# Optimization experiments

Hardware: AMD Instinct MI355X
Metric: run time of the kernel (lower is better)

Reference implementation:

```python
import jax, jax.numpy as jnp
import numpy as np

N = 8192
D = 1024
TIME_DECAY = 86400.0
EPS = 1e-10


def setup_inputs() -> dict:
    key = jax.random.key(0)
    ks = jax.random.split(key, 8)
    x = jax.random.normal(ks[0], (N, D), dtype=jnp.float32)
    # timestamps spanning ~10 days so decay bias is non-trivial
    timestamps = jax.random.uniform(ks[1], (N,), dtype=jnp.float32) * (10.0 * TIME_DECAY)
    s = 1.0 / np.sqrt(D)
    Wq = jax.random.normal(ks[2], (D, D), dtype=jnp.float32) * s
    bq = jnp.zeros((D,), dtype=jnp.float32)
    Wk = jax.random.normal(ks[3], (D, D), dtype=jnp.float32) * s
    bk = jnp.zeros((D,), dtype=jnp.float32)
    Wv = jax.random.normal(ks[4], (D, D), dtype=jnp.float32) * s
    bv = jnp.zeros((D,), dtype=jnp.float32)
    return {"x": x, "timestamps": timestamps, "Wq": Wq, "bq": bq,
            "Wk": Wk, "bk": bk, "Wv": Wv, "bv": bv}


def reference(x, timestamps, Wq, bq, Wk, bk, Wv, bv):
    scale = jnp.asarray(D ** 0.5, x.dtype)
    # torch nn.Linear: y = x @ W.T + b
    Q = x @ Wq.T + bq          # [N, D]
    K = x @ Wk.T + bk          # [N, D]
    V = x @ Wv.T + bv          # [N, D]
    time_diff = timestamps[:, None] - timestamps[None, :]   # [N, N]
    time_decay = jnp.exp(-jnp.abs(time_diff) / TIME_DECAY)  # [N, N]
    scores = (Q @ K.T) / scale + jnp.log(time_decay + EPS)  # [N, N]
    attn = jax.nn.softmax(scores, axis=-1)
    return attn @ V
```

## Files before the change

### kernel.cpp

```cpp
#include <hip/hip_runtime.h>


using half8   = __attribute__((ext_vector_type(8))) _Float16;
using half4   = __attribute__((ext_vector_type(4))) _Float16;
using floatx4 = __attribute__((ext_vector_type(4))) float;

__device__ __forceinline__ void gload_lds16(const void* g, void* l) {
  __builtin_amdgcn_global_load_lds((const __attribute__((address_space(1))) void*)g,
                                   (__attribute__((address_space(3))) void*)l,
                                   16, 0, 0);
}

template<int N> __device__ __forceinline__ void waitv() {
  if constexpr (N == 12)      asm volatile("s_waitcnt vmcnt(12)" ::: "memory");
  else if constexpr (N == 9)  asm volatile("s_waitcnt vmcnt(9)"  ::: "memory");
  else if constexpr (N == 8)  asm volatile("s_waitcnt vmcnt(8)"  ::: "memory");
  else if constexpr (N == 6)  asm volatile("s_waitcnt vmcnt(6)"  ::: "memory");
  else if constexpr (N == 4)  asm volatile("s_waitcnt vmcnt(4)"  ::: "memory");
  else if constexpr (N == 3)  asm volatile("s_waitcnt vmcnt(3)"  ::: "memory");
  else                        asm volatile("s_waitcnt vmcnt(0)"  ::: "memory");
}

template<int BM, int BN, int WM, int WN, int MI, int NJ>
__device__ __forceinline__ void kloop_ring(
    const _Float16* __restrict__ A, const _Float16* __restrict__ B,
    long rowBase, long colBase, int lda, int ldb, int K,
    _Float16* __restrict__ As, _Float16* __restrict__ Bs,
    floatx4 (&acc)[MI][NJ])
{
  constexpr int LA = BM / 128, LB = BN / 128;
  constexpr int ISS = LA + LB;
  const int tid = threadIdx.x;
  const int w = tid >> 6, lane = tid & 63;
  const int q = lane >> 4, l15 = lane & 15;
  const int wr = w / WN, wcn = w & (WN - 1);

  const int sc = (((lane & 3) ^ ((lane >> 3) & 3)) << 3);
  const _Float16* Agp[LA]; int Aoff[LA];
  const _Float16* Bgp[LB]; int Boff[LB];
#pragma unroll
  for (int p = 0; p < LA; ++p) {
    const int row = ((w * (BM * 4) + p * 512 + lane * 8) >> 5);
    Agp[p] = A + (rowBase + row) * (long)lda + sc;
    Aoff[p] = w * (BM * 4) + p * 512;
  }
#pragma unroll
  for (int p = 0; p < LB; ++p) {
    const int row = ((w * (BN * 4) + p * 512 + lane * 8) >> 5);
    Bgp[p] = B + (colBase + row) * (long)ldb + sc;
    Boff[p] = w * (BN * 4) + p * 512;
  }

  const int pRd   = (q ^ ((l15 >> 1) & 3)) << 3;
  const int aBase = (wr * (BM / WM) + l15) * 32 + pRd;
  const int bBase = (wcn * (BN / WN) + l15) * 32 + pRd;

  auto issue = [&](int t) {
    const int s = t & 3;
    const long ko = (long)t * 32;
    _Float16* Asl = As + s * (BM * 32);
    _Float16* Bsl = Bs + s * (BN * 32);
#pragma unroll
    for (int p = 0; p < LA; ++p) gload_lds16(Agp[p] + ko, Asl + Aoff[p]);
#pragma unroll
    for (int p = 0; p < LB; ++p) gload_lds16(Bgp[p] + ko, Bsl + Boff[p]);
  };

  auto compute = [&](int slot) {
    const _Float16* Asl = As + slot * (BM * 32);
    const _Float16* Bsl = Bs + slot * (BN * 32);
    half8 bfr[NJ], afr[MI];
#pragma unroll
    for (int j = 0; j < NJ; ++j) bfr[j] = *(const half8*)&Bsl[bBase + j * 512];
#pragma unroll
    for (int i = 0; i < MI; ++i) afr[i] = *(const half8*)&Asl[aBase + i * 512];
    __builtin_amdgcn_s_setprio(1);
#pragma unroll
    for (int i = 0; i < MI; ++i)
#pragma unroll
      for (int j = 0; j < NJ; ++j)
        acc[i][j] = __builtin_amdgcn_mfma_f32_16x16x32_f16(afr[i], bfr[j], acc[i][j], 0, 0, 0);
    __builtin_amdgcn_s_setprio(0);
  };

  const int NT = K >> 5;
  issue(0); issue(1); issue(2);
  for (int t = 0; t < NT - 3; ++t) {
    issue(t + 3);
    waitv<3 * ISS>();
    __builtin_amdgcn_s_barrier();
    compute(t & 3);
    __builtin_amdgcn_s_barrier();
  }
  waitv<2 * ISS>(); __builtin_amdgcn_s_barrier();
  compute((NT - 3) & 3);          __builtin_amdgcn_s_barrier();
  waitv<1 * ISS>(); __builtin_amdgcn_s_barrier();
  compute((NT - 2) & 3);          __builtin_amdgcn_s_barrier();
  waitv<0>();       __builtin_amdgcn_s_barrier();
  compute((NT - 1) & 3);
}

template<int BM, int BN, int WM, int WN, int BIAS_MODE, int OUT_MODE, int SWZ>
__global__ __launch_bounds__(512, 2)
void gemm256_k(const _Float16* __restrict__ A, const _Float16* __restrict__ B,
               void* __restrict__ Cout, const float* __restrict__ bias,
               int lda, int ldb, int ldc, int K, float outScale)
{
  constexpr int MI = BM / WM / 16, NJ = BN / WN / 16;
  __shared__ __align__(16) _Float16 As[4 * BM * 32];
  __shared__ __align__(16) _Float16 Bs[4 * BN * 32];

  int tx, ty;
  if (SWZ) {
    const int bflat = blockIdx.y * gridDim.x + blockIdx.x;
    ty = bflat % gridDim.y;
    tx = bflat / gridDim.y;
  } else {
    tx = blockIdx.x; ty = blockIdx.y;
  }
  const long rowBase = (long)ty * BM;
  const long colBase = (long)tx * BN;

  floatx4 acc[MI][NJ] = {};
  kloop_ring<BM, BN, WM, WN, MI, NJ>(A, B, rowBase, colBase, lda, ldb, K, As, Bs, acc);

  const int tid = threadIdx.x;
  const int w = tid >> 6, lane = tid & 63;
  const int q = lane >> 4, l15 = lane & 15;
  const int wr = w / WN, wcn = w & (WN - 1);
#pragma unroll
  for (int i = 0; i < MI; ++i) {
#pragma unroll
    for (int r = 0; r < 4; ++r) {
      const long rowg = rowBase + wr * (BM / WM) + 16 * i + q * 4 + r;
#pragma unroll
      for (int j = 0; j < NJ; ++j) {
        const long colg = colBase + wcn * (BN / WN) + 16 * j + l15;
        float v = acc[i][j][r];
        if (BIAS_MODE == 1) v += bias[colg];
        if (BIAS_MODE == 2) v += bias[rowg];
        if (BIAS_MODE == 3) v *= bias[rowg];
        v *= outScale;
        if (OUT_MODE == 2) ((float*)Cout)[rowg * ldc + colg] = v;
        else               ((_Float16*)Cout)[rowg * ldc + colg] = (_Float16)v;
      }
    }
  }
}

__global__ __launch_bounds__(512, 2)
void gemm_stats256_k(const _Float16* __restrict__ A, const _Float16* __restrict__ B,
                     const float* __restrict__ ts, _Float16* __restrict__ U,
                     float* __restrict__ part, int lda, int ldb, int N, int K,
                     float qkScale)
{
  constexpr int BM = 256, BN = 256, WM = 2, WN = 4, MI = 8, NJ = 4;
  __shared__ __align__(16) _Float16 As[4 * BM * 32];
  __shared__ __align__(16) _Float16 Bs[4 * BN * 32];
  __shared__ float trs[256], tcs[256];
  __shared__ float sL[2][4][128];
  const int tid = threadIdx.x;
  const long rowBase = (long)blockIdx.y * 256;
  const long colBase = (long)blockIdx.x * 256;

  if (tid < 256) {
    trs[tid] = ts[rowBase + tid];
    tcs[tid] = ts[colBase + tid];
  }

  floatx4 acc[MI][NJ] = {};
  kloop_ring<BM, BN, WM, WN, MI, NJ>(A, B, rowBase, colBase, lda, ldb, K, As, Bs, acc);

  const int w = tid >> 6, lane = tid & 63;
  const int q = lane >> 4, l15 = lane & 15;
  const int wr = w >> 2, wcn = w & 3;
  const float inv_td = 1.0f / 86400.0f;
#pragma unroll
  for (int i = 0; i < 8; ++i) {
#pragma unroll
    for (int r = 0; r < 4; ++r) {
      const int rowl = wr * 128 + 16 * i + q * 4 + r;
      const float tr = trs[rowl];
      float ls = 0.0f;
#pragma unroll
      for (int j = 0; j < 4; ++j) {
        const int coll = wcn * 64 + 16 * j + l15;
        const float sv = acc[i][j][r] * qkScale
                       - fabsf(tr - tcs[coll]) * inv_td - 4.0f;
        const float u = __expf(sv);
        ls += u;
        U[(rowBase + rowl) * (long)N + (colBase + coll)] = (_Float16)u;
      }
      for (int mask = 1; mask <= 8; mask <<= 1)
        ls += __shfl_xor(ls, mask, 64);
      if (l15 == 0) sL[wr][wcn][16 * i + 4 * q + r] = ls;
    }
  }
  __syncthreads();
  if (tid < 256) {
    const int wr2 = tid >> 7, rl = tid & 127;
    part[(rowBase + tid) * 32 + blockIdx.x] =
        sL[wr2][0][rl] + sL[wr2][1][rl] + sL[wr2][2][rl] + sL[wr2][3][rl];
  }
}

__global__ void combine_k(const float* __restrict__ part, float* __restrict__ invL) {
  const int r = blockIdx.x * 256 + threadIdx.x;
  float L = 0.0f;
  for (int c = 0; c < 32; ++c) L += part[(long)r * 32 + c];
  invL[r] = 1.0f / L;
}

__global__ void cvt_k(const float* __restrict__ in, _Float16* __restrict__ out, int n) {
  const int i = (blockIdx.x * 256 + threadIdx.x) * 4;
  if (i >= n) return;
  const float4 v = *(const float4*)(in + i);
  half4 o = { (_Float16)v.x, (_Float16)v.y, (_Float16)v.z, (_Float16)v.w };
  *(half4*)(out + i) = o;
}

extern "C" void kernel_launch(void* const* d_in, const int* in_sizes, int n_in,
                              void* d_out, int out_size, void* d_ws, size_t ws_size,
                              hipStream_t stream)
{
  (void)in_sizes; (void)n_in; (void)out_size; (void)ws_size;
  const int N = 8192, D = 1024;
  const float* x  = (const float*)d_in[0];
  const float* ts = (const float*)d_in[1];
  const float* Wq = (const float*)d_in[2];
  const float* bq = (const float*)d_in[3];
  const float* Wk = (const float*)d_in[4];
  const float* bk = (const float*)d_in[5];
  const float* Wv = (const float*)d_in[6];
  const float* bv = (const float*)d_in[7];

  char* p = (char*)d_ws;
  auto grab = [&](size_t bytes) {
    char* r = p;
    p += (bytes + 255) & ~(size_t)255;
    return r;
  };
  _Float16* xh    = (_Float16*)grab((size_t)N * D * 2);
  _Float16* wqkh  = (_Float16*)grab((size_t)2 * D * D * 2);
  _Float16* wvh   = (_Float16*)grab((size_t)D * D * 2);
  _Float16* QKcat = (_Float16*)grab((size_t)N * 2 * D * 2);
  _Float16* VTh   = (_Float16*)grab((size_t)D * N * 2);
  _Float16* Uh    = (_Float16*)grab((size_t)N * N * 2);
  float*    part  = (float*)grab((size_t)N * 32 * sizeof(float));
  float*    invL  = (float*)grab((size_t)N * sizeof(float));
  float*    bcat  = (float*)grab((size_t)2 * D * sizeof(float));

  cvt_k<<<N * D / 1024, 256, 0, stream>>>(x,  xh,  N * D);
  cvt_k<<<D * D / 1024, 256, 0, stream>>>(Wq, wqkh,         D * D);
  cvt_k<<<D * D / 1024, 256, 0, stream>>>(Wk, wqkh + D * D, D * D);
  cvt_k<<<D * D / 1024, 256, 0, stream>>>(Wv, wvh, D * D);
  hipMemcpyAsync(bcat,     bq, D * sizeof(float), hipMemcpyDeviceToDevice, stream);
  hipMemcpyAsync(bcat + D, bk, D * sizeof(float), hipMemcpyDeviceToDevice, stream);

  dim3 blk(512);
  gemm256_k<256, 256, 2, 4, 1, 0, 0><<<dim3(2 * D / 256, N / 256), blk, 0, stream>>>(
      xh, wqkh, QKcat, bcat, D, D, 2 * D, D, 1.0f);
  gemm256_k<128, 256, 2, 4, 2, 0, 0><<<dim3(N / 256, D / 128), blk, 0, stream>>>(
      wvh, xh, VTh, bv, D, D, N, D, 1.0f);
  gemm_stats256_k<<<dim3(N / 256, N / 256), blk, 0, stream>>>(
      QKcat, QKcat + D, ts, Uh, part, 2 * D, 2 * D, N, D, 1.0f / 32.0f);
  combine_k<<<N / 256, 256, 0, stream>>>(part, invL);
  gemm256_k<256, 128, 4, 2, 3, 2, 1><<<dim3(D / 128, N / 256), blk, 0, stream>>>(
      Uh, VTh, d_out, invL, N, N, D, N, 1.0f);
}
```

Baseline: 555.0 us.

## Switch GEMM k-loop to 64-wide K tiles with 2/3-slot LDS pipeline

Replaces the 4-slot ring with K-step 32 by a K-step-64 loop using a new XOR swizzle and either double or triple buffering, selected by a template parameter. Each stage now runs two MFMA sub-steps per barrier pair, which halves the number of barriers and waits per K. The V-projection GEMM also changes its tile shape to 256x128. The cost is less prefetch depth and different LDS use per block, which could expose more load latency.

After: 494.0 us. 1.12x faster.

```diff
diff --git a/kernel.cpp b/kernel.cpp
--- a/kernel.cpp
+++ b/kernel.cpp
@@ -12,103 +12,119 @@
 }
 
 template<int N> __device__ __forceinline__ void waitv() {
-  if constexpr (N == 12)      asm volatile("s_waitcnt vmcnt(12)" ::: "memory");
-  else if constexpr (N == 9)  asm volatile("s_waitcnt vmcnt(9)"  ::: "memory");
-  else if constexpr (N == 8)  asm volatile("s_waitcnt vmcnt(8)"  ::: "memory");
-  else if constexpr (N == 6)  asm volatile("s_waitcnt vmcnt(6)"  ::: "memory");
-  else if constexpr (N == 4)  asm volatile("s_waitcnt vmcnt(4)"  ::: "memory");
-  else if constexpr (N == 3)  asm volatile("s_waitcnt vmcnt(3)"  ::: "memory");
-  else                        asm volatile("s_waitcnt vmcnt(0)"  ::: "memory");
-}
-
-template<int BM, int BN, int WM, int WN, int MI, int NJ>
-__device__ __forceinline__ void kloop_ring(
+  if constexpr (N == 12)     asm volatile("s_waitcnt vmcnt(12)" ::: "memory");
+  else if constexpr (N == 8) asm volatile("s_waitcnt vmcnt(8)"  ::: "memory");
+  else if constexpr (N == 6) asm volatile("s_waitcnt vmcnt(6)"  ::: "memory");
+  else                       asm volatile("s_waitcnt vmcnt(0)"  ::: "memory");
+}
+
+template<int BM, int BN, int WM, int WN, int SLOTS, int MI, int NJ>
+__device__ __forceinline__ void kloop64(
     const _Float16* __restrict__ A, const _Float16* __restrict__ B,
     long rowBase, long colBase, int lda, int ldb, int K,
     _Float16* __restrict__ As, _Float16* __restrict__ Bs,
     floatx4 (&acc)[MI][NJ])
 {
-  constexpr int LA = BM / 128, LB = BN / 128;
+  static_assert(MI == BM / WM / 16 && NJ == BN / WN / 16);
+  constexpr int LA = BM / 64, LB = BN / 64;
   constexpr int ISS = LA + LB;
   const int tid = threadIdx.x;
   const int w = tid >> 6, lane = tid & 63;
   const int q = lane >> 4, l15 = lane & 15;
   const int wr = w / WN, wcn = w & (WN - 1);
 
-  const int sc = (((lane & 3) ^ ((lane >> 3) & 3)) << 3);
-  const _Float16* Agp[LA]; int Aoff[LA];
-  const _Float16* Bgp[LB]; int Boff[LB];
-#pragma unroll
-  for (int p = 0; p < LA; ++p) {
-    const int row = ((w * (BM * 4) + p * 512 + lane * 8) >> 5);
-    Agp[p] = A + (rowBase + row) * (long)lda + sc;
-    Aoff[p] = w * (BM * 4) + p * 512;
-  }
-#pragma unroll
-  for (int p = 0; p < LB; ++p) {
-    const int row = ((w * (BN * 4) + p * 512 + lane * 8) >> 5);
-    Bgp[p] = B + (colBase + row) * (long)ldb + sc;
-    Boff[p] = w * (BN * 4) + p * 512;
-  }
-
-  const int pRd   = (q ^ ((l15 >> 1) & 3)) << 3;
-  const int aBase = (wr * (BM / WM) + l15) * 32 + pRd;
-  const int bBase = (wcn * (BN / WN) + l15) * 32 + pRd;
-
-  auto issue = [&](int t) {
-    const int s = t & 3;
-    const long ko = (long)t * 32;
-    _Float16* Asl = As + s * (BM * 32);
-    _Float16* Bsl = Bs + s * (BN * 32);
-#pragma unroll
-    for (int p = 0; p < LA; ++p) gload_lds16(Agp[p] + ko, Asl + Aoff[p]);
-#pragma unroll
-    for (int p = 0; p < LB; ++p) gload_lds16(Bgp[p] + ko, Bsl + Boff[p]);
+  const int sc = ((lane & 7) ^ (lane >> 3)) << 3;
+  const _Float16* Agp[LA]; const _Float16* Bgp[LB];
+#pragma unroll
+  for (int p = 0; p < LA; ++p)
+    Agp[p] = A + (rowBase + p * 64 + (tid >> 3)) * (long)lda + sc;
+#pragma unroll
+  for (int p = 0; p < LB; ++p)
+    Bgp[p] = B + (colBase + p * 64 + (tid >> 3)) * (long)ldb + sc;
+  const int ldsOff = tid * 8;
+
+  const int aRow = wr * (BM / WM) + l15;
+  const int bRow = wcn * (BN / WN) + l15;
+  const int cx = l15 & 7;
+
+  auto issue = [&](int t, int slot) {
+    const int ko = t << 6;
+    _Float16* Asl = As + slot * (BM * 64);
+    _Float16* Bsl = Bs + slot * (BN * 64);
+#pragma unroll
+    for (int p = 0; p < LA; ++p) gload_lds16(Agp[p] + ko, Asl + p * 4096 + ldsOff);
+#pragma unroll
+    for (int p = 0; p < LB; ++p) gload_lds16(Bgp[p] + ko, Bsl + p * 4096 + ldsOff);
   };
 
   auto compute = [&](int slot) {
-    const _Float16* Asl = As + slot * (BM * 32);
-    const _Float16* Bsl = Bs + slot * (BN * 32);
-    half8 bfr[NJ], afr[MI];
-#pragma unroll
-    for (int j = 0; j < NJ; ++j) bfr[j] = *(const half8*)&Bsl[bBase + j * 512];
-#pragma unroll
-    for (int i = 0; i < MI; ++i) afr[i] = *(const half8*)&Asl[aBase + i * 512];
-    __builtin_amdgcn_s_setprio(1);
-#pragma unroll
-    for (int i = 0; i < MI; ++i)
+    const _Float16* Asl = As + slot * (BM * 64);
+    const _Float16* Bsl = Bs + slot * (BN * 64);
+#pragma unroll
+    for (int kk = 0; kk < 2; ++kk) {
+      const int pc = ((kk * 4 + q) ^ cx) << 3;
+      half8 bfr[NJ];
 #pragma unroll
       for (int j = 0; j < NJ; ++j)
-        acc[i][j] = __builtin_amdgcn_mfma_f32_16x16x32_f16(afr[i], bfr[j], acc[i][j], 0, 0, 0);
-    __builtin_amdgcn_s_setprio(0);
+        bfr[j] = *(const half8*)&Bsl[(bRow + 16 * j) * 64 + pc];
+      half8 afr[MI];
+#pragma unroll
+      for (int i = 0; i < MI; ++i)
+        afr[i] = *(const half8*)&Asl[(aRow + 16 * i) * 64 + pc];
+      __builtin_amdgcn_s_setprio(1);
+#pragma unroll
+      for (int i = 0; i < MI; ++i)
+#pragma unroll
+        for (int j = 0; j < NJ; ++j)
+          acc[i][j] = __builtin_amdgcn_mfma_f32_16x16x32_f16(afr[i], bfr[j], acc[i][j], 0, 0, 0);
+      __builtin_amdgcn_s_setprio(0);
+    }
   };
 
-  const int NT = K >> 5;
-  issue(0); issue(1); issue(2);
-  for (int t = 0; t < NT - 3; ++t) {
-    issue(t + 3);
-    waitv<3 * ISS>();
-    __builtin_amdgcn_s_barrier();
-    compute(t & 3);
-    __builtin_amdgcn_s_barrier();
-  }
-  waitv<2 * ISS>(); __builtin_amdgcn_s_barrier();
-  compute((NT - 3) & 3);          __builtin_amdgcn_s_barrier();
-  waitv<1 * ISS>(); __builtin_amdgcn_s_barrier();
-  compute((NT - 2) & 3);          __builtin_amdgcn_s_barrier();
-  waitv<0>();       __builtin_amdgcn_s_barrier();
-  compute((NT - 1) & 3);
-}
-
-template<int BM, int BN, int WM, int WN, int BIAS_MODE, int OUT_MODE, int SWZ>
+  const int NT = K >> 6;
+  if constexpr (SLOTS == 2) {
+    issue(0, 0);
+    int cs = 0;
+    for (int t = 0; t < NT - 1; ++t) {
+      issue(t + 1, cs ^ 1);
+      waitv<ISS>();
+      __builtin_amdgcn_s_barrier();
+      compute(cs);
+      __builtin_amdgcn_s_barrier();
+      cs ^= 1;
+    }
+    waitv<0>(); __builtin_amdgcn_s_barrier();
+    compute(cs);
+  } else {
+    static_assert(SLOTS == 3);
+    issue(0, 0); issue(1, 1);
+    int cs = 0, is = 2;
+    for (int t = 0; t < NT - 2; ++t) {
+      issue(t + 2, is);
+      waitv<2 * ISS>();
+      __builtin_amdgcn_s_barrier();
+      compute(cs);
+      __builtin_amdgcn_s_barrier();
+      cs = (cs == 2) ? 0 : cs + 1;
+      is = (is == 2) ? 0 : is + 1;
+    }
+    waitv<ISS>(); __builtin_amdgcn_s_barrier();
+    compute(cs);  __builtin_amdgcn_s_barrier();
+    cs = (cs == 2) ? 0 : cs + 1;
+    waitv<0>();   __builtin_amdgcn_s_barrier();
+    compute(cs);
+  }
+}
+
+template<int BM, int BN, int WM, int WN, int SLOTS, int BIAS_MODE, int OUT_MODE, int SWZ>
 __global__ __launch_bounds__(512, 2)
 void gemm256_k(const _Float16* __restrict__ A, const _Float16* __restrict__ B,
                void* __restrict__ Cout, const float* __restrict__ bias,
                int lda, int ldb, int ldc, int K, float outScale)
 {
   constexpr int MI = BM / WM / 16, NJ = BN / WN / 16;
-  __shared__ __align__(16) _Float16 As[4 * BM * 32];
-  __shared__ __align__(16) _Float16 Bs[4 * BN * 32];
+  __shared__ __align__(16) _Float16 As[SLOTS * BM * 64];
+  __shared__ __align__(16) _Float16 Bs[SLOTS * BN * 64];
 
   int tx, ty;
   if (SWZ) {
@@ -122,7 +138,7 @@
   const long colBase = (long)tx * BN;
 
   floatx4 acc[MI][NJ] = {};
-  kloop_ring<BM, BN, WM, WN, MI, NJ>(A, B, rowBase, colBase, lda, ldb, K, As, Bs, acc);
+  kloop64<BM, BN, WM, WN, SLOTS, MI, NJ>(A, B, rowBase, colBase, lda, ldb, K, As, Bs, acc);
 
   const int tid = threadIdx.x;
   const int w = tid >> 6, lane = tid & 63;
@@ -155,8 +171,8 @@
                      float qkScale)
 {
   constexpr int BM = 256, BN = 256, WM = 2, WN = 4, MI = 8, NJ = 4;
-  __shared__ __align__(16) _Float16 As[4 * BM * 32];
-  __shared__ __align__(16) _Float16 Bs[4 * BN * 32];
+  __shared__ __align__(16) _Float16 As[2 * BM * 64];
+  __shared__ __align__(16) _Float16 Bs[2 * BN * 64];
   __shared__ float trs[256], tcs[256];
   __shared__ float sL[2][4][128];
   const int tid = threadIdx.x;
@@ -169,7 +185,7 @@
   }
 
   floatx4 acc[MI][NJ] = {};
-  kloop_ring<BM, BN, WM, WN, MI, NJ>(A, B, rowBase, colBase, lda, ldb, K, As, Bs, acc);
+  kloop64<BM, BN, WM, WN, 2, MI, NJ>(A, B, rowBase, colBase, lda, ldb, K, As, Bs, acc);
 
   const int w = tid >> 6, lane = tid & 63;
   const int q = lane >> 4, l15 = lane & 15;
@@ -258,13 +274,13 @@
   hipMemcpyAsync(bcat + D, bk, D * sizeof(float), hipMemcpyDeviceToDevice, stream);
 
   dim3 blk(512);
-  gemm256_k<256, 256, 2, 4, 1, 0, 0><<<dim3(2 * D / 256, N / 256), blk, 0, stream>>>(
+  gemm256_k<256, 256, 2, 4, 2, 1, 0, 0><<<dim3(2 * D / 256, N / 256), blk, 0, stream>>>(
       xh, wqkh, QKcat, bcat, D, D, 2 * D, D, 1.0f);
-  gemm256_k<128, 256, 2, 4, 2, 0, 0><<<dim3(N / 256, D / 128), blk, 0, stream>>>(
+  gemm256_k<256, 128, 4, 2, 3, 2, 0, 0><<<dim3(N / 128, D / 256), blk, 0, stream>>>(
       wvh, xh, VTh, bv, D, D, N, D, 1.0f);
   gemm_stats256_k<<<dim3(N / 256, N / 256), blk, 0, stream>>>(
       QKcat, QKcat + D, ts, Uh, part, 2 * D, 2 * D, N, D, 1.0f / 32.0f);
   combine_k<<<N / 256, 256, 0, stream>>>(part, invL);
-  gemm256_k<256, 128, 4, 2, 3, 2, 1><<<dim3(D / 128, N / 256), blk, 0, stream>>>(
+  gemm256_k<256, 128, 4, 2, 3, 3, 2, 1><<<dim3(D / 128, N / 256), blk, 0, stream>>>(
       Uh, VTh, d_out, invL, N, N, D, N, 1.0f);
 }
```
